# Performance work log

Hardware: AMD Instinct MI355X
Metric: run time of the kernel (lower is better)

Reference implementation:

```python
import jax, jax.numpy as jnp
import numpy as np

NUM_EXPERTS = 8
INPUT_SIZE = 2048
OUTPUT_SIZE = 8192
EXPERT_SIZES = np.array([3000, 5000, 4096, 2048, 6000, 4000, 4624, 4000], dtype=np.int64)  # sums to 32768
TOTAL_TOKENS = int(EXPERT_SIZES.sum())


def setup_inputs() -> dict:
    key = jax.random.key(0)
    k_in, k_w = jax.random.split(key)
    inputs = jax.random.normal(k_in, (TOTAL_TOKENS, INPUT_SIZE), dtype=jnp.float32)
    # per-expert Linear weights, torch layout [out, in]
    weights = jax.random.normal(k_w, (NUM_EXPERTS, OUTPUT_SIZE, INPUT_SIZE), dtype=jnp.float32) * 0.02
    expert_size = jnp.asarray(EXPERT_SIZES)
    return {"inputs": inputs, "weights": weights, "expert_size": expert_size}


def reference(inputs, weights, expert_size):
    # Grouped GEMM: split tokens by static per-expert counts, y_i = x_i @ W_i^T, concat.
    sizes = [int(s) for s in np.asarray(expert_size)]
    offsets = np.concatenate([[0], np.cumsum(sizes)])
    outs = []
    for i in range(len(sizes)):
        x_i = inputs[offsets[i]:offsets[i + 1]]  # [n_i, input_size]
        outs.append(jnp.einsum('ti,oi->to', x_i, weights[i]))  # [n_i, output_size]
    return jnp.concatenate(outs, axis=0)  # [total_tokens, output_size]
```

## Files before the change

kernel.cpp:

```cpp
#include <hip/hip_runtime.h>

typedef __bf16 bf16x8 __attribute__((ext_vector_type(8)));
typedef float  f32x4  __attribute__((ext_vector_type(4)));

#define KDIM 2048
#define NDIM 8192
#define MTOT 32768
#define BM 256
#define BN 256
#define BK 64
#define NT 32
#define NMT 131
#define NWG (NMT * 32)
#define ABUF (BM * BK)
#define BBUF (BN * BK)

__device__ __forceinline__ void gload_lds16(const void* g, void* l) {
    __builtin_amdgcn_global_load_lds(
        (const __attribute__((address_space(1))) void*)g,
        (__attribute__((address_space(3))) void*)l, 16, 0, 0);
}

__global__ __launch_bounds__(256) void convert_f32_bf16(
    const float* __restrict__ src, __bf16* __restrict__ dst, int n8)
{
    const int stride = gridDim.x * blockDim.x;
    for (int i = blockIdx.x * blockDim.x + threadIdx.x; i < n8; i += stride) {
        const f32x4* p = (const f32x4*)(src + (size_t)i * 8);
        f32x4 a = p[0], b = p[1];
        bf16x8 h;
        #pragma unroll
        for (int j = 0; j < 4; ++j) { h[j] = (__bf16)a[j]; h[4 + j] = (__bf16)b[j]; }
        *(bf16x8*)(dst + (size_t)i * 8) = h;
    }
}

__global__ void __launch_bounds__(512, 2) moe_gemm_1b(
    const __bf16* __restrict__ A,
    const __bf16* __restrict__ W,
    float* __restrict__ C)
{
    __shared__ __bf16 AsF[3 * ABUF];
    __shared__ __bf16 BsF[2 * BBUF];

    const int tstart[9] = {0, 12, 32, 48, 56, 80, 96, 115, 131};
    const int offs[9]   = {0, 3000, 8000, 12096, 14144, 20144, 24144, 28768, 32768};

    const int bid = blockIdx.x;
    const int mt = bid >> 5;
    const int nt = bid & 31;

    int e = 0;
    #pragma unroll
    for (int i = 1; i < 8; ++i) e += (mt >= tstart[i]) ? 1 : 0;
    const int row0 = offs[e] + (mt - tstart[e]) * BM;
    int rows = offs[e + 1] - row0;
    if (rows > BM) rows = BM;
    const int col0 = nt * BN;

    const int tid  = threadIdx.x;
    const int lane = tid & 63;
    const int w    = tid >> 6;
    const int wm   = w >> 2;
    const int wn   = w & 3;

    const int lrow = lane >> 3;
    const int csrc = ((lane & 7) ^ lrow) * 8;

    const __bf16 *aX[2], *aY[2], *b0[2], *b1[2];
    int ldsAX[2], ldsAY[2], ldsB0[2], ldsB1[2];
    #pragma unroll
    for (int c = 0; c < 2; ++c) {
        const int q  = w * 2 + c;
        const int tX = q * 8 + (q & 8) * 8;
        const int tY = tX + 64;
        int rX = tX + lrow; rX = (rX < rows) ? rX : 0;
        int rY = tY + lrow; rY = (rY < rows) ? rY : 0;
        aX[c] = A + (size_t)(row0 + rX) * KDIM + csrc;
        aY[c] = A + (size_t)(row0 + rY) * KDIM + csrc;
        b0[c] = W + (size_t)(e * NDIM + col0 + q * 8 + lrow) * KDIM + csrc;
        b1[c] = W + (size_t)(e * NDIM + col0 + 128 + q * 8 + lrow) * KDIM + csrc;
        ldsAX[c] = tX * BK;
        ldsAY[c] = tY * BK;
        ldsB0[c] = (q * 8) * BK;
        ldsB1[c] = (128 + q * 8) * BK;
    }

#define STAGE_A(ab, o) { \
    gload_lds16(aX[0] + (o), &AsF[(ab) * ABUF + ldsAX[0]]); \
    gload_lds16(aX[1] + (o), &AsF[(ab) * ABUF + ldsAX[1]]); \
    gload_lds16(aY[0] + (o), &AsF[(ab) * ABUF + ldsAY[0]]); \
    gload_lds16(aY[1] + (o), &AsF[(ab) * ABUF + ldsAY[1]]); }
#define STAGE_B(bb, o) { \
    gload_lds16(b0[0] + (o), &BsF[(bb) * BBUF + ldsB0[0]]); \
    gload_lds16(b0[1] + (o), &BsF[(bb) * BBUF + ldsB0[1]]); \
    gload_lds16(b1[0] + (o), &BsF[(bb) * BBUF + ldsB1[0]]); \
    gload_lds16(b1[1] + (o), &BsF[(bb) * BBUF + ldsB1[1]]); }

    const int frow = lane & 15;
    const int g8   = (lane >> 4) * 8;
    const int swc  = (frow & 7) << 3;
    const int ck0  = g8 ^ swc;
    const int ck1  = (32 + g8) ^ swc;
    const int arow = wm * 128 + frow;
    const int brow = wn * 64 + frow;

    f32x4 acc[8][4];
    #pragma unroll
    for (int m = 0; m < 8; ++m)
        #pragma unroll
        for (int n = 0; n < 4; ++n)
            acc[m][n] = (f32x4){0.f, 0.f, 0.f, 0.f};

    bf16x8 bk0[4], bk1[4];
    bf16x8 av0[4], av1[4];

#define RD_B(bb) { _Pragma("unroll") for (int n = 0; n < 4; ++n) { \
        bk0[n] = *(const bf16x8*)&BsF[(bb) * BBUF + (brow + n * 16) * BK + ck0]; \
        bk1[n] = *(const bf16x8*)&BsF[(bb) * BBUF + (brow + n * 16) * BK + ck1]; } }

#define RD_A(ab, h) { _Pragma("unroll") for (int mm = 0; mm < 4; ++mm) { \
        av0[mm] = *(const bf16x8*)&AsF[(ab) * ABUF + (arow + (4 * (h) + mm) * 16) * BK + ck0]; \
        av1[mm] = *(const bf16x8*)&AsF[(ab) * ABUF + (arow + (4 * (h) + mm) * 16) * BK + ck1]; } }

#define MFMA_CL(h) { \
    __builtin_amdgcn_s_setprio(1); \
    _Pragma("unroll") for (int mm = 0; mm < 4; ++mm) \
        _Pragma("unroll") for (int n = 0; n < 4; ++n) \
            acc[4 * (h) + mm][n] = __builtin_amdgcn_mfma_f32_16x16x32_bf16( \
                av0[mm], bk0[n], acc[4 * (h) + mm][n], 0, 0, 0); \
    _Pragma("unroll") for (int mm = 0; mm < 4; ++mm) \
        _Pragma("unroll") for (int n = 0; n < 4; ++n) \
            acc[4 * (h) + mm][n] = __builtin_amdgcn_mfma_f32_16x16x32_bf16( \
                av1[mm], bk1[n], acc[4 * (h) + mm][n], 0, 0, 0); \
    __builtin_amdgcn_s_setprio(0); }

#define FENCE asm volatile("" ::: "memory")

    STAGE_A(0, 0); STAGE_B(0, 0);
    STAGE_A(1, BK);
    asm volatile("s_waitcnt vmcnt(4)" ::: "memory");
    __builtin_amdgcn_s_barrier();

    int a0i = 0;
    int b0i = 0;
    #pragma unroll 1
    for (int i = 0; i < NT; ++i) {
        int a2i = a0i + 2; if (a2i >= 3) a2i -= 3;
        int t1 = i + 1; if (t1 > NT - 1) t1 = NT - 1;
        int t2 = i + 2; if (t2 > NT - 1) t2 = NT - 1;

        FENCE;
        RD_B(b0i);
        RD_A(a0i, 0);
        STAGE_B(b0i ^ 1, t1 * BK);
        STAGE_A(a2i, t2 * BK);
        MFMA_CL(0);
        RD_A(a0i, 1);
        MFMA_CL(1);
        asm volatile("s_waitcnt vmcnt(4)" ::: "memory");
        __builtin_amdgcn_s_barrier();

        a0i = a0i + 1; if (a0i >= 3) a0i -= 3;
        b0i ^= 1;
    }

    const int crow = (lane >> 4) * 4;
    const int ccol = lane & 15;
    #pragma unroll
    for (int m = 0; m < 8; ++m) {
        #pragma unroll
        for (int j2 = 0; j2 < 4; ++j2) {
            const int r = wm * 128 + m * 16 + crow + j2;
            if (r < rows) {
                float* dst = C + (size_t)(row0 + r) * NDIM + col0 + wn * 64 + ccol;
                #pragma unroll
                for (int n = 0; n < 4; ++n)
                    dst[n * 16] = acc[m][n][j2];
            }
        }
    }
#undef STAGE_A
#undef STAGE_B
#undef RD_B
#undef RD_A
#undef MFMA_CL
#undef FENCE
}

__global__ __launch_bounds__(256) void moe_gemm_f32(
    const float* __restrict__ A, const float* __restrict__ W, float* __restrict__ C)
{
    __shared__ __bf16 Asb[128][64];
    __shared__ __bf16 Bsb[128][64];

    const int tstart[9] = {0, 24, 64, 96, 112, 159, 191, 228, 260};
    const int offs[9]   = {0, 3000, 8000, 12096, 14144, 20144, 24144, 28768, 32768};

    const int mt = blockIdx.y;
    int e = 0;
    #pragma unroll
    for (int i = 1; i < 8; ++i) e += (mt >= tstart[i]) ? 1 : 0;
    const int row0 = offs[e] + (mt - tstart[e]) * 128;
    int rows = offs[e + 1] - row0;
    if (rows > 128) rows = 128;
    const int col0 = blockIdx.x * 128;

    const float* __restrict__ Abase = A + (size_t)row0 * KDIM;
    const float* __restrict__ Wbase = W + ((size_t)e * NDIM + (size_t)col0) * KDIM;

    const int tid  = threadIdx.x;
    const int lane = tid & 63;
    const int wid  = tid >> 6;
    const int wr   = (wid >> 1) * 64;
    const int wc   = (wid & 1) * 64;
    const int srow = tid >> 2;
    const int scol = (tid & 3) * 16;

    f32x4 acc[4][4];
    #pragma unroll
    for (int m = 0; m < 4; ++m)
        #pragma unroll
        for (int n = 0; n < 4; ++n)
            acc[m][n] = (f32x4){0.f, 0.f, 0.f, 0.f};
    const f32x4 fzero = (f32x4){0.f, 0.f, 0.f, 0.f};

    for (int k0 = 0; k0 < KDIM; k0 += 64) {
        __syncthreads();
        #pragma unroll
        for (int rr = 0; rr < 2; ++rr) {
            const int r = srow + rr * 64;
            {
                const bool valid = (r < rows);
                const float* pa = Abase + (size_t)r * KDIM + k0 + scol;
                f32x4 v[4];
                #pragma unroll
                for (int i = 0; i < 4; ++i) v[i] = valid ? *(const f32x4*)(pa + 4 * i) : fzero;
                bf16x8 h0, h1;
                #pragma unroll
                for (int i = 0; i < 8; ++i) {
                    h0[i] = (__bf16)v[i >> 2][i & 3];
                    h1[i] = (__bf16)v[2 + (i >> 2)][i & 3];
                }
                *((bf16x8*)&Asb[r][scol]) = h0;
                *((bf16x8*)&Asb[r][scol + 8]) = h1;
            }
            {
                const float* pb = Wbase + (size_t)r * KDIM + k0 + scol;
                f32x4 v[4];
                #pragma unroll
                for (int i = 0; i < 4; ++i) v[i] = *(const f32x4*)(pb + 4 * i);
                bf16x8 h0, h1;
                #pragma unroll
                for (int i = 0; i < 8; ++i) {
                    h0[i] = (__bf16)v[i >> 2][i & 3];
                    h1[i] = (__bf16)v[2 + (i >> 2)][i & 3];
                }
                *((bf16x8*)&Bsb[r][scol]) = h0;
                *((bf16x8*)&Bsb[r][scol + 8]) = h1;
            }
        }
        __syncthreads();
        #pragma unroll
        for (int ks = 0; ks < 2; ++ks) {
            const int kb = ks * 32 + (lane >> 4) * 8;
            bf16x8 af[4], bfr[4];
            #pragma unroll
            for (int m = 0; m < 4; ++m)
                af[m] = *((const bf16x8*)&Asb[wr + m * 16 + (lane & 15)][kb]);
            #pragma unroll
            for (int n = 0; n < 4; ++n)
                bfr[n] = *((const bf16x8*)&Bsb[wc + n * 16 + (lane & 15)][kb]);
            #pragma unroll
            for (int m = 0; m < 4; ++m)
                #pragma unroll
                for (int n = 0; n < 4; ++n)
                    acc[m][n] = __builtin_amdgcn_mfma_f32_16x16x32_bf16(
                        af[m], bfr[n], acc[m][n], 0, 0, 0);
        }
    }

    const int crow = (lane >> 4) * 4;
    const int ccol = lane & 15;
    #pragma unroll
    for (int m = 0; m < 4; ++m) {
        #pragma unroll
        for (int j = 0; j < 4; ++j) {
            const int r = wr + m * 16 + crow + j;
            if (r < rows) {
                float* dst = C + (size_t)(row0 + r) * NDIM + col0 + wc + ccol;
                #pragma unroll
                for (int n = 0; n < 4; ++n)
                    dst[n * 16] = acc[m][n][j];
            }
        }
    }
}

extern "C" void kernel_launch(void* const* d_in, const int* in_sizes, int n_in,
                              void* d_out, int out_size, void* d_ws, size_t ws_size,
                              hipStream_t stream) {
    const float* A = (const float*)d_in[0];
    const float* W = (const float*)d_in[1];
    float* C = (float*)d_out;

    const size_t nA = (size_t)MTOT * KDIM;
    const size_t nW = (size_t)8 * NDIM * KDIM;
    const size_t WS_NEED = (nA + nW) * 2;

    if (ws_size >= WS_NEED) {
        __bf16* Abf = (__bf16*)d_ws;
        __bf16* Wbf = (__bf16*)((char*)d_ws + nA * 2);
        hipLaunchKernelGGL(convert_f32_bf16, dim3(2048), dim3(256), 0, stream,
                           A, Abf, (int)(nA / 8));
        hipLaunchKernelGGL(convert_f32_bf16, dim3(2048), dim3(256), 0, stream,
                           W, Wbf, (int)(nW / 8));
        hipLaunchKernelGGL(moe_gemm_1b, dim3(NWG), dim3(512), 0, stream,
                           Abf, Wbf, C);
    } else {
        hipLaunchKernelGGL(moe_gemm_f32, dim3(NDIM / 128, 260), dim3(256), 0, stream,
                           A, W, C);
    }
}
```

Before: 1.434 ms.

## Load A fragments directly from global memory into registers, bypassing LDS

Removes the triple-buffered LDS staging for the A (token) tile. Each wave now reads its A fragments straight from global memory into registers every K-step, while B keeps its double-buffered LDS path. This cuts LDS use per block, which may allow more blocks per CU, and drops the A LDS reads. In exchange, each A tile is read four times (once per N-wave) through the caches, and the A global loads are issued in the same iteration they are consumed, so their latency is no longer hidden by prefetch.

```diff
diff --git a/kernel.cpp b/kernel.cpp
--- a/kernel.cpp
+++ b/kernel.cpp
@@ -12,7 +12,6 @@
 #define NT 32
 #define NMT 131
 #define NWG (NMT * 32)
-#define ABUF (BM * BK)
 #define BBUF (BN * BK)
 
 __device__ __forceinline__ void gload_lds16(const void* g, void* l) {
@@ -35,12 +34,11 @@
     }
 }
 
-__global__ void __launch_bounds__(512, 2) moe_gemm_1b(
+__global__ void __launch_bounds__(512, 2) moe_gemm_ga(
     const __bf16* __restrict__ A,
     const __bf16* __restrict__ W,
     float* __restrict__ C)
 {
-    __shared__ __bf16 AsF[3 * ABUF];
     __shared__ __bf16 BsF[2 * BBUF];
 
     const int tstart[9] = {0, 12, 32, 48, 56, 80, 96, 115, 131};
@@ -67,30 +65,17 @@
     const int lrow = lane >> 3;
     const int csrc = ((lane & 7) ^ lrow) * 8;
 
-    const __bf16 *aX[2], *aY[2], *b0[2], *b1[2];
-    int ldsAX[2], ldsAY[2], ldsB0[2], ldsB1[2];
+    const __bf16 *b0[2], *b1[2];
+    int ldsB0[2], ldsB1[2];
     #pragma unroll
     for (int c = 0; c < 2; ++c) {
-        const int q  = w * 2 + c;
-        const int tX = q * 8 + (q & 8) * 8;
-        const int tY = tX + 64;
-        int rX = tX + lrow; rX = (rX < rows) ? rX : 0;
-        int rY = tY + lrow; rY = (rY < rows) ? rY : 0;
-        aX[c] = A + (size_t)(row0 + rX) * KDIM + csrc;
-        aY[c] = A + (size_t)(row0 + rY) * KDIM + csrc;
+        const int q = w * 2 + c;
         b0[c] = W + (size_t)(e * NDIM + col0 + q * 8 + lrow) * KDIM + csrc;
         b1[c] = W + (size_t)(e * NDIM + col0 + 128 + q * 8 + lrow) * KDIM + csrc;
-        ldsAX[c] = tX * BK;
-        ldsAY[c] = tY * BK;
         ldsB0[c] = (q * 8) * BK;
         ldsB1[c] = (128 + q * 8) * BK;
     }
 
-#define STAGE_A(ab, o) { \
-    gload_lds16(aX[0] + (o), &AsF[(ab) * ABUF + ldsAX[0]]); \
-    gload_lds16(aX[1] + (o), &AsF[(ab) * ABUF + ldsAX[1]]); \
-    gload_lds16(aY[0] + (o), &AsF[(ab) * ABUF + ldsAY[0]]); \
-    gload_lds16(aY[1] + (o), &AsF[(ab) * ABUF + ldsAY[1]]); }
 #define STAGE_B(bb, o) { \
     gload_lds16(b0[0] + (o), &BsF[(bb) * BBUF + ldsB0[0]]); \
     gload_lds16(b0[1] + (o), &BsF[(bb) * BBUF + ldsB0[1]]); \
@@ -102,8 +87,16 @@
     const int swc  = (frow & 7) << 3;
     const int ck0  = g8 ^ swc;
     const int ck1  = (32 + g8) ^ swc;
+    const int brow = wn * 64 + frow;
     const int arow = wm * 128 + frow;
-    const int brow = wn * 64 + frow;
+
+    const __bf16* aP[8];
+    #pragma unroll
+    for (int mf = 0; mf < 8; ++mf) {
+        int r = arow + mf * 16;
+        r = (r < rows) ? r : 0;
+        aP[mf] = A + (size_t)(row0 + r) * KDIM + g8;
+    }
 
     f32x4 acc[8][4];
     #pragma unroll
@@ -113,56 +106,48 @@
             acc[m][n] = (f32x4){0.f, 0.f, 0.f, 0.f};
 
     bf16x8 bk0[4], bk1[4];
-    bf16x8 av0[4], av1[4];
+    bf16x8 aA0[4], aA1[4];
+    bf16x8 aB0[4], aB1[4];
 
 #define RD_B(bb) { _Pragma("unroll") for (int n = 0; n < 4; ++n) { \
         bk0[n] = *(const bf16x8*)&BsF[(bb) * BBUF + (brow + n * 16) * BK + ck0]; \
         bk1[n] = *(const bf16x8*)&BsF[(bb) * BBUF + (brow + n * 16) * BK + ck1]; } }
 
-#define RD_A(ab, h) { _Pragma("unroll") for (int mm = 0; mm < 4; ++mm) { \
-        av0[mm] = *(const bf16x8*)&AsF[(ab) * ABUF + (arow + (4 * (h) + mm) * 16) * BK + ck0]; \
-        av1[mm] = *(const bf16x8*)&AsF[(ab) * ABUF + (arow + (4 * (h) + mm) * 16) * BK + ck1]; } }
-
-#define MFMA_CL(h) { \
+#define GA(d0, d1, h, ko) { _Pragma("unroll") for (int mm = 0; mm < 4; ++mm) { \
+        d0[mm] = *(const bf16x8*)(aP[4 * (h) + mm] + (ko)); \
+        d1[mm] = *(const bf16x8*)(aP[4 * (h) + mm] + (ko) + 32); } }
+
+#define MFMA_CL(h, a0, a1) { \
     __builtin_amdgcn_s_setprio(1); \
     _Pragma("unroll") for (int mm = 0; mm < 4; ++mm) \
         _Pragma("unroll") for (int n = 0; n < 4; ++n) \
             acc[4 * (h) + mm][n] = __builtin_amdgcn_mfma_f32_16x16x32_bf16( \
-                av0[mm], bk0[n], acc[4 * (h) + mm][n], 0, 0, 0); \
+                a0[mm], bk0[n], acc[4 * (h) + mm][n], 0, 0, 0); \
     _Pragma("unroll") for (int mm = 0; mm < 4; ++mm) \
         _Pragma("unroll") for (int n = 0; n < 4; ++n) \
             acc[4 * (h) + mm][n] = __builtin_amdgcn_mfma_f32_16x16x32_bf16( \
-                av1[mm], bk1[n], acc[4 * (h) + mm][n], 0, 0, 0); \
+                a1[mm], bk1[n], acc[4 * (h) + mm][n], 0, 0, 0); \
     __builtin_amdgcn_s_setprio(0); }
 
 #define FENCE asm volatile("" ::: "memory")
 
-    STAGE_A(0, 0); STAGE_B(0, 0);
-    STAGE_A(1, BK);
-    asm volatile("s_waitcnt vmcnt(4)" ::: "memory");
+    STAGE_B(0, 0);
+    asm volatile("s_waitcnt vmcnt(0)" ::: "memory");
     __builtin_amdgcn_s_barrier();
 
-    int a0i = 0;
-    int b0i = 0;
     #pragma unroll 1
     for (int i = 0; i < NT; ++i) {
-        int a2i = a0i + 2; if (a2i >= 3) a2i -= 3;
         int t1 = i + 1; if (t1 > NT - 1) t1 = NT - 1;
-        int t2 = i + 2; if (t2 > NT - 1) t2 = NT - 1;
+        const int ko = i * BK;
 
         FENCE;
-        RD_B(b0i);
-        RD_A(a0i, 0);
-        STAGE_B(b0i ^ 1, t1 * BK);
-        STAGE_A(a2i, t2 * BK);
-        MFMA_CL(0);
-        RD_A(a0i, 1);
-        MFMA_CL(1);
-        asm volatile("s_waitcnt vmcnt(4)" ::: "memory");
+        RD_B(i & 1);
+        GA(aA0, aA1, 0, ko);
+        STAGE_B((i + 1) & 1, t1 * BK);
+        GA(aB0, aB1, 1, ko);
+        MFMA_CL(0, aA0, aA1);
+        MFMA_CL(1, aB0, aB1);
         __builtin_amdgcn_s_barrier();
-
-        a0i = a0i + 1; if (a0i >= 3) a0i -= 3;
-        b0i ^= 1;
     }
 
     const int crow = (lane >> 4) * 4;
@@ -180,10 +165,9 @@
             }
         }
     }
-#undef STAGE_A
 #undef STAGE_B
 #undef RD_B
-#undef RD_A
+#undef GA
 #undef MFMA_CL
 #undef FENCE
 }
@@ -315,7 +299,7 @@
                            A, Abf, (int)(nA / 8));
         hipLaunchKernelGGL(convert_f32_bf16, dim3(2048), dim3(256), 0, stream,
                            W, Wbf, (int)(nW / 8));
-        hipLaunchKernelGGL(moe_gemm_1b, dim3(NWG), dim3(512), 0, stream,
+        hipLaunchKernelGGL(moe_gemm_ga, dim3(NWG), dim3(512), 0, stream,
                            Abf, Wbf, C);
     } else {
         hipLaunchKernelGGL(moe_gemm_f32, dim3(NDIM / 128, 260), dim3(256), 0, stream,
```

Result: slower. 2.851 ms (+98.8%).
